# Optimization experiments

Measured on AMD Instinct MI355X. Metric: run time of the kernel, lower is better.

Reference implementation:

```python
import jax, jax.numpy as jnp
import numpy as np

HIDDEN_DIM = 640
VOCAB_SIZE = 1024


def setup_inputs() -> dict:
    key = jax.random.key(0)
    kf, kp, kw, kb = jax.random.split(key, 4)
    B, T, U, H, V = 8, 256, 64, HIDDEN_DIM, VOCAB_SIZE
    f = jax.random.normal(kf, (B, T, H), dtype=jnp.float32)
    p = jax.random.normal(kp, (B, U, H), dtype=jnp.float32)
    # nn.Linear default init: U(-1/sqrt(H), 1/sqrt(H))
    bound = 1.0 / np.sqrt(H)
    W = jax.random.uniform(kw, (V, H), minval=-bound, maxval=bound, dtype=jnp.float32)
    b = jax.random.uniform(kb, (V,), minval=-bound, maxval=bound, dtype=jnp.float32)
    return {"f": f, "p": p, "W": W, "b": b}


def reference(f, p, W, b):
    # f: (B,T,H), p: (B,U,H) -> combined: (B,T,U,H)
    combined = f[:, :, None, :] + p[:, None, :, :]
    h = jax.nn.relu(combined)
    # Linear: h @ W^T + b -> (B,T,U,V)
    logits = jnp.einsum('btuh,vh->btuv', h, W) + b
    return logits
```

## Files before the change

kernel.cpp:

```cpp
#include <hip/hip_runtime.h>
#include <hip/hip_bf16.h>

#define BDIM 8
#define TDIM 256
#define UDIM 64
#define HDIM 640
#define VDIM 1024
#define MDIM (BDIM * TDIM * UDIM)

#define BK 32
#define NT (HDIM / BK)
#define NKC (HDIM / 8)
#define GSTRIDE (NKC * 128)

typedef __attribute__((ext_vector_type(8))) short short8;
typedef __attribute__((ext_vector_type(4))) float f32x4;

__device__ __forceinline__ ushort f2bf(float x) {
    union { float f; unsigned int u; } v; v.f = x;
    unsigned int r = (v.u + 0x7fffu + ((v.u >> 16) & 1u)) >> 16;
    return (ushort)r;
}


__global__ __launch_bounds__(256) void cvt_w_tiled_kernel(
    const float* __restrict__ W, ushort* __restrict__ Wt)
{
    const int c  = blockIdx.x * 256 + threadIdx.x;
    const int lr = c & 15;
    const int q  = c >> 4;
    const int kc = q % NKC;
    const int g  = q / NKC;
    const int v  = g * 16 + lr;
    const float* src = W + (size_t)v * HDIM + kc * 8;
    f32x4 w0 = *(const f32x4*)src;
    f32x4 w1 = *(const f32x4*)(src + 4);
    short8 o;
    #pragma unroll
    for (int e = 0; e < 4; ++e) {
        o[e]     = (short)f2bf(w0[e]);
        o[e + 4] = (short)f2bf(w1[e]);
    }
    *(short8*)(Wt + (size_t)c * 8) = o;
}

__global__ __launch_bounds__(256) void build_h_tiled_kernel(
    const float* __restrict__ f, const float* __restrict__ p,
    ushort* __restrict__ ht)
{
    const int c  = blockIdx.x * 256 + threadIdx.x;
    const int lr = c & 15;
    const int q  = c >> 4;
    const int kc = q % NKC;
    const int g  = q / NKC;
    const int m  = g * 16 + lr;
    const int b  = m >> 14;
    const int t  = (m >> 6) & (TDIM - 1);
    const int u  = m & (UDIM - 1);
    const int k  = kc * 8;
    const float* fr = f + (size_t)(b * TDIM + t) * HDIM + k;
    const float* pr = p + (size_t)(b * UDIM + u) * HDIM + k;
    f32x4 f0 = *(const f32x4*)fr;
    f32x4 f1 = *(const f32x4*)(fr + 4);
    f32x4 p0 = *(const f32x4*)pr;
    f32x4 p1 = *(const f32x4*)(pr + 4);
    short8 o;
    #pragma unroll
    for (int e = 0; e < 4; ++e) {
        float a0 = fmaxf(f0[e] + p0[e], 0.0f);
        float a1 = fmaxf(f1[e] + p1[e], 0.0f);
        o[e]     = (short)f2bf(a0);
        o[e + 4] = (short)f2bf(a1);
    }
    *(short8*)(ht + (size_t)c * 8) = o;
}

#define GLDS(srcptr, ldsptr)                                                   \
    __builtin_amdgcn_global_load_lds(                                          \
        (const __attribute__((address_space(1))) void*)(srcptr),               \
        (__attribute__((address_space(3))) void*)(ldsptr), 16, 0, 0)

__global__ __launch_bounds__(256, 2) void hgemm_frag_kernel(
    const ushort* __restrict__ ht,
    const ushort* __restrict__ Wt,
    const float* __restrict__ bias,
    float* __restrict__ out)
{
    __shared__ ushort Sh[2][12288];

    const int tid  = threadIdx.x;
    const int lane = tid & 63;
    const int wave = tid >> 6;
    const int wm   = wave >> 1;
    const int wn   = wave & 1;

    const int bid   = blockIdx.x;
    const int work  = (bid & 7) * 512 + (bid >> 3);
    const int mtile = work >> 3;
    const int ntile = work & 7;
    const int m0 = mtile * 256;
    const int v0 = ntile * 128;

    const int gA0 = mtile * 16;
    const int gB0 = ntile * 8;
    const int la  = lane * 8;

    const ushort* sbase[6];
    int doff[6];
    #pragma unroll
    for (int i = 0; i < 6; ++i) {
        const int q = wave * 6 + i;
        if (q < 16) {
            sbase[i] = ht + (size_t)(gA0 + q) * GSTRIDE + la;
            doff[i]  = q * 512;
        } else {
            sbase[i] = Wt + (size_t)(gB0 + (q - 16)) * GSTRIDE + la;
            doff[i]  = 8192 + (q - 16) * 512;
        }
    }

    f32x4 acc[8][4];
    #pragma unroll
    for (int i = 0; i < 8; ++i)
        #pragma unroll
        for (int j = 0; j < 4; ++j)
            acc[i][j] = (f32x4)0.0f;

#define STG(kt, bf) do {                                                       \
        _Pragma("unroll")                                                      \
        for (int i_ = 0; i_ < 6; ++i_)                                         \
            GLDS(sbase[i_] + (kt) * 512, &Sh[bf][doff[i_]]);                   \
    } while (0)

#define TILE(t, d) do {                                                        \
        if ((t) + 1 < NT) {                                                    \
            STG((t) + 1, (d) ^ 1);                                             \
            asm volatile("s_waitcnt vmcnt(6)" ::: "memory");                   \
        } else {                                                               \
            asm volatile("s_waitcnt vmcnt(0)" ::: "memory");                   \
        }                                                                      \
        __builtin_amdgcn_sched_barrier(0);                                     \
        __builtin_amdgcn_s_barrier();         \
        __builtin_amdgcn_sched_barrier(0);                                     \
        short8 afr[8], bfr[4];                                                 \
        _Pragma("unroll")                                                      \
        for (int mi = 0; mi < 8; ++mi)                                         \
            afr[mi] = *(const short8*)(&Sh[d][(wm * 8 + mi) * 512 + la]);      \
        _Pragma("unroll")                                                      \
        for (int ni = 0; ni < 4; ++ni)                                         \
            bfr[ni] = *(const short8*)(&Sh[d][8192 + (wn * 4 + ni) * 512 + la]);\
        __builtin_amdgcn_s_setprio(1);                                         \
        _Pragma("unroll")                                                      \
        for (int mi = 0; mi < 8; ++mi)                                         \
            _Pragma("unroll")                                                  \
            for (int ni = 0; ni < 4; ++ni)                                     \
                acc[mi][ni] = __builtin_amdgcn_mfma_f32_16x16x32_bf16(         \
                    afr[mi], bfr[ni], acc[mi][ni], 0, 0, 0);                   \
        __builtin_amdgcn_s_setprio(0);                                         \
        __builtin_amdgcn_sched_barrier(0);                                     \
        __builtin_amdgcn_s_barrier();              \
    } while (0)

    STG(0, 0);
    #pragma unroll 1
    for (int t = 0; t < NT; t += 2) {
        TILE(t, 0);
        TILE(t + 1, 1);
    }
#undef TILE
#undef STG

    const int lr = lane & 15;
    #pragma unroll
    for (int ni = 0; ni < 4; ++ni) {
        const int col = v0 + wn * 64 + ni * 16 + lr;
        const float bv = bias[col];
        #pragma unroll
        for (int mi = 0; mi < 8; ++mi) {
            const int rbase = m0 + wm * 128 + mi * 16 + ((lane >> 4) << 2);
            #pragma unroll
            for (int reg = 0; reg < 4; ++reg) {
                out[(size_t)(rbase + reg) * VDIM + col] = acc[mi][ni][reg] + bv;
            }
        }
    }
}

__global__ void cvt_w_kernel(const float* __restrict__ W, ushort* __restrict__ Wb) {
    int i = (blockIdx.x * 256 + threadIdx.x) * 4;
    f32x4 w = *(const f32x4*)(W + i);
    ushort4 o;
    o.x = f2bf(w[0]); o.y = f2bf(w[1]); o.z = f2bf(w[2]); o.w = f2bf(w[3]);
    *(ushort4*)(Wb + i) = o;
}

template <bool USE_WB>
__global__ __launch_bounds__(256) void joint_gemm_kernel(
    const float* __restrict__ f, const float* __restrict__ p,
    const float* __restrict__ Wf, const ushort* __restrict__ Wb,
    const float* __restrict__ bias, float* __restrict__ out)
{
    __shared__ ushort Alds[128 * 64];
    __shared__ ushort Blds[128 * 64];

    const int tid  = threadIdx.x;
    const int lane = tid & 63;
    const int wave = tid >> 6;
    const int wm   = wave >> 1;
    const int wn   = wave & 1;

    const int bid   = blockIdx.x;
    const int work  = (bid & 7) * 1024 + (bid >> 3);
    const int mtile = work >> 3;
    const int ntile = work & 7;
    const int m0 = mtile * 128;
    const int v0 = ntile * 128;

    const int b  = m0 >> 14;
    const int t0 = (m0 >> 6) & (TDIM - 1);

    const float*  fbase = f + (size_t)(b * TDIM + t0) * HDIM;
    const float*  pbase = p + (size_t)b * UDIM * HDIM;
    const ushort* wbbase = Wb + (size_t)v0 * HDIM;
    const float*  wfbase = Wf + (size_t)v0 * HDIM;

    f32x4 acc[4][4];
    #pragma unroll
    for (int i = 0; i < 4; ++i)
        #pragma unroll
        for (int j = 0; j < 4; ++j)
            acc[i][j] = (f32x4)0.0f;

    for (int kt = 0; kt < HDIM / 64; ++kt) {
        const int k0 = kt * 64;
        __syncthreads();

        if (USE_WB) {
            #pragma unroll
            for (int it = 0; it < 4; ++it) {
                const int c   = it * 256 + tid;
                const int row = c >> 3;
                const int j   = c & 7;
                const ushort* src = wbbase + row * HDIM + k0 + ((j ^ (row & 7)) << 3);
                GLDS(src, &Blds[(it * 256 + wave * 64) * 8]);
            }
        } else {
            #pragma unroll
            for (int it = 0; it < 4; ++it) {
                const int c   = it * 256 + tid;
                const int row = c >> 3;
                const int j   = c & 7;
                const float* wp = wfbase + row * HDIM + k0 + j * 8;
                f32x4 w0 = *(const f32x4*)wp;
                f32x4 w1 = *(const f32x4*)(wp + 4);
                short8 wv;
                #pragma unroll
                for (int e = 0; e < 4; ++e) {
                    wv[e]     = (short)f2bf(w0[e]);
                    wv[e + 4] = (short)f2bf(w1[e]);
                }
                *(short8*)(&Blds[(row * 8 + (j ^ (row & 7))) * 8]) = wv;
            }
        }

        #pragma unroll
        for (int it = 0; it < 4; ++it) {
            const int c   = it * 256 + tid;
            const int row = c >> 3;
            const int j   = c & 7;
            const float* fp_ = fbase + (row >> 6) * HDIM + k0 + j * 8;
            const float* pp_ = pbase + (row & 63) * HDIM + k0 + j * 8;
            f32x4 f0 = *(const f32x4*)fp_;
            f32x4 f1 = *(const f32x4*)(fp_ + 4);
            f32x4 p0 = *(const f32x4*)pp_;
            f32x4 p1 = *(const f32x4*)(pp_ + 4);
            short8 hv;
            #pragma unroll
            for (int e = 0; e < 4; ++e) {
                float a0 = fmaxf(f0[e] + p0[e], 0.0f);
                float a1 = fmaxf(f1[e] + p1[e], 0.0f);
                hv[e]     = (short)f2bf(a0);
                hv[e + 4] = (short)f2bf(a1);
            }
            *(short8*)(&Alds[(row * 8 + (j ^ (row & 7))) * 8]) = hv;
        }

        __syncthreads();

        #pragma unroll
        for (int ks = 0; ks < 2; ++ks) {
            short8 afr[4], bfr[4];
            #pragma unroll
            for (int mi = 0; mi < 4; ++mi) {
                const int r = wm * 64 + mi * 16 + (lane & 15);
                const int j = ks * 4 + (lane >> 4);
                afr[mi] = *(const short8*)(&Alds[(r * 8 + (j ^ (r & 7))) * 8]);
            }
            #pragma unroll
            for (int ni = 0; ni < 4; ++ni) {
                const int r = wn * 64 + ni * 16 + (lane & 15);
                const int j = ks * 4 + (lane >> 4);
                bfr[ni] = *(const short8*)(&Blds[(r * 8 + (j ^ (r & 7))) * 8]);
            }
            #pragma unroll
            for (int mi = 0; mi < 4; ++mi)
                #pragma unroll
                for (int ni = 0; ni < 4; ++ni)
                    acc[mi][ni] = __builtin_amdgcn_mfma_f32_16x16x32_bf16(
                        afr[mi], bfr[ni], acc[mi][ni], 0, 0, 0);
        }
    }

    #pragma unroll
    for (int ni = 0; ni < 4; ++ni) {
        const int col = v0 + wn * 64 + ni * 16 + (lane & 15);
        const float bv = bias[col];
        #pragma unroll
        for (int mi = 0; mi < 4; ++mi) {
            const int rbase = m0 + wm * 64 + mi * 16 + ((lane >> 4) << 2);
            #pragma unroll
            for (int reg = 0; reg < 4; ++reg) {
                out[(size_t)(rbase + reg) * VDIM + col] = acc[mi][ni][reg] + bv;
            }
        }
    }
}

extern "C" void kernel_launch(void* const* d_in, const int* in_sizes, int n_in,
                              void* d_out, int out_size, void* d_ws, size_t ws_size,
                              hipStream_t stream) {
    const float* f    = (const float*)d_in[0];
    const float* p    = (const float*)d_in[1];
    const float* W    = (const float*)d_in[2];
    const float* bias = (const float*)d_in[3];
    float* out = (float*)d_out;

    const size_t wb_bytes = (size_t)VDIM * HDIM * sizeof(ushort);
    const size_t h_bytes  = (size_t)MDIM * HDIM * sizeof(ushort);

    if (ws_size >= wb_bytes + h_bytes) {
        ushort* Wt = (ushort*)d_ws;
        ushort* ht = (ushort*)((char*)d_ws + wb_bytes);
        cvt_w_tiled_kernel<<<(VDIM * HDIM / 8) / 256, 256, 0, stream>>>(W, Wt);
        build_h_tiled_kernel<<<(MDIM / 256) * (HDIM / 8), 256, 0, stream>>>(f, p, ht);
        const int grid = (MDIM / 256) * (VDIM / 128);
        hgemm_frag_kernel<<<grid, 256, 0, stream>>>(ht, Wt, bias, out);
    } else if (ws_size >= wb_bytes) {
        ushort* Wb = (ushort*)d_ws;
        cvt_w_kernel<<<(VDIM * HDIM) / 1024, 256, 0, stream>>>(W, Wb);
        joint_gemm_kernel<true><<<(MDIM / 128) * (VDIM / 128), 256, 0, stream>>>(
            f, p, W, Wb, bias, out);
    } else {
        joint_gemm_kernel<false><<<(MDIM / 128) * (VDIM / 128), 256, 0, stream>>>(
            f, p, W, nullptr, bias, out);
    }
}
```

Before: 408.4 us.

## Use triple-buffered LDS ring to prefetch two K-tiles ahead with one barrier

Replaces the double-buffered K loop in the bf16 GEMM with a three-slot LDS ring. Two tiles are prefetched up front, and each iteration issues the load for tile t+2 after reading fragments from slot t. This drops the second barrier per iteration and gives each load more time to arrive. LDS use grows from 48KB to 72KB per block, which with two blocks per CU (144KB) should still fit in the 160KB LDS of MI355X, but it raises pressure. The correctness of reusing a slot without a trailing barrier depends on fragment reads finishing before the next overwrite.

```diff
diff --git a/kernel.cpp b/kernel.cpp
--- a/kernel.cpp
+++ b/kernel.cpp
@@ -80,13 +80,13 @@
         (const __attribute__((address_space(1))) void*)(srcptr),               \
         (__attribute__((address_space(3))) void*)(ldsptr), 16, 0, 0)
 
-__global__ __launch_bounds__(256, 2) void hgemm_frag_kernel(
+__global__ __launch_bounds__(256, 2) void hgemm_ring_kernel(
     const ushort* __restrict__ ht,
     const ushort* __restrict__ Wt,
     const float* __restrict__ bias,
     float* __restrict__ out)
 {
-    __shared__ ushort Sh[2][12288];
+    __shared__ ushort Sh[3][12288];
 
     const int tid  = threadIdx.x;
     const int lane = tid & 63;
@@ -132,42 +132,42 @@
             GLDS(sbase[i_] + (kt) * 512, &Sh[bf][doff[i_]]);                   \
     } while (0)
 
-#define TILE(t, d) do {                                                        \
-        if ((t) + 1 < NT) {                                                    \
-            STG((t) + 1, (d) ^ 1);                                             \
-            asm volatile("s_waitcnt vmcnt(6)" ::: "memory");                   \
-        } else {                                                               \
-            asm volatile("s_waitcnt vmcnt(0)" ::: "memory");                   \
-        }                                                                      \
-        __builtin_amdgcn_sched_barrier(0);                                     \
-        __builtin_amdgcn_s_barrier();         \
-        __builtin_amdgcn_sched_barrier(0);                                     \
-        short8 afr[8], bfr[4];                                                 \
-        _Pragma("unroll")                                                      \
-        for (int mi = 0; mi < 8; ++mi)                                         \
-            afr[mi] = *(const short8*)(&Sh[d][(wm * 8 + mi) * 512 + la]);      \
-        _Pragma("unroll")                                                      \
-        for (int ni = 0; ni < 4; ++ni)                                         \
-            bfr[ni] = *(const short8*)(&Sh[d][8192 + (wn * 4 + ni) * 512 + la]);\
-        __builtin_amdgcn_s_setprio(1);                                         \
-        _Pragma("unroll")                                                      \
-        for (int mi = 0; mi < 8; ++mi)                                         \
-            _Pragma("unroll")                                                  \
-            for (int ni = 0; ni < 4; ++ni)                                     \
-                acc[mi][ni] = __builtin_amdgcn_mfma_f32_16x16x32_bf16(         \
-                    afr[mi], bfr[ni], acc[mi][ni], 0, 0, 0);                   \
-        __builtin_amdgcn_s_setprio(0);                                         \
-        __builtin_amdgcn_sched_barrier(0);                                     \
-        __builtin_amdgcn_s_barrier();              \
-    } while (0)
-
     STG(0, 0);
+    STG(1, 1);
+
+    int d = 0;
+    int e = 2;
     #pragma unroll 1
-    for (int t = 0; t < NT; t += 2) {
-        TILE(t, 0);
-        TILE(t + 1, 1);
-    }
-#undef TILE
+    for (int t = 0; t < NT; ++t) {
+        if (t < NT - 1) { asm volatile("s_waitcnt vmcnt(6)" ::: "memory"); }
+        else            { asm volatile("s_waitcnt vmcnt(0)" ::: "memory"); }
+        __builtin_amdgcn_sched_barrier(0);
+        __builtin_amdgcn_s_barrier();
+        __builtin_amdgcn_sched_barrier(0);
+
+        short8 afr[8], bfr[4];
+        #pragma unroll
+        for (int mi = 0; mi < 8; ++mi)
+            afr[mi] = *(const short8*)(&Sh[d][(wm * 8 + mi) * 512 + la]);
+        #pragma unroll
+        for (int ni = 0; ni < 4; ++ni)
+            bfr[ni] = *(const short8*)(&Sh[d][8192 + (wn * 4 + ni) * 512 + la]);
+
+        if (t + 2 < NT) STG(t + 2, e);
+
+        __builtin_amdgcn_s_setprio(1);
+        #pragma unroll
+        for (int mi = 0; mi < 8; ++mi)
+            #pragma unroll
+            for (int ni = 0; ni < 4; ++ni)
+                acc[mi][ni] = __builtin_amdgcn_mfma_f32_16x16x32_bf16(
+                    afr[mi], bfr[ni], acc[mi][ni], 0, 0, 0);
+        __builtin_amdgcn_s_setprio(0);
+        __builtin_amdgcn_sched_barrier(0);
+
+        d = (d == 2) ? 0 : d + 1;
+        e = (e == 2) ? 0 : e + 1;
+    }
 #undef STG
 
     const int lr = lane & 15;
@@ -344,7 +344,7 @@
         cvt_w_tiled_kernel<<<(VDIM * HDIM / 8) / 256, 256, 0, stream>>>(W, Wt);
         build_h_tiled_kernel<<<(MDIM / 256) * (HDIM / 8), 256, 0, stream>>>(f, p, ht);
         const int grid = (MDIM / 256) * (VDIM / 128);
-        hgemm_frag_kernel<<<grid, 256, 0, stream>>>(ht, Wt, bias, out);
+        hgemm_ring_kernel<<<grid, 256, 0, stream>>>(ht, Wt, bias, out);
     } else if (ws_size >= wb_bytes) {
         ushort* Wb = (ushort*)d_ws;
         cvt_w_kernel<<<(VDIM * HDIM) / 1024, 256, 0, stream>>>(W, Wb);
```

Measured after the change: 398.9 us. 1.02x faster.
